# Optimization experiments

Hardware: AMD Instinct MI355X
Metric: run time of the kernel (lower is better)

## Reference

```python
import jax, jax.numpy as jnp
import numpy as np

B, S, D, H = 8, 384, 768, 12
MAX_POS = 512
P = 2 * MAX_POS - 1  # 1023


def setup_inputs() -> dict:
    key = jax.random.key(0)
    ks = jax.random.split(key, 14)
    w = 0.02
    return {
        "x": jax.random.normal(ks[0], (B, S, D), jnp.float32),
        "rel_pos_emb": jax.random.normal(ks[1], (P, D), jnp.float32),
        "Wq": jax.random.normal(ks[2], (D, D), jnp.float32) * w,
        "bq": jax.random.normal(ks[3], (D,), jnp.float32) * w,
        "Wk": jax.random.normal(ks[4], (D, D), jnp.float32) * w,
        "bk": jax.random.normal(ks[5], (D,), jnp.float32) * w,
        "Wv": jax.random.normal(ks[6], (D, D), jnp.float32) * w,
        "bv": jax.random.normal(ks[7], (D,), jnp.float32) * w,
        "q_bias": jax.random.normal(ks[8], (D,), jnp.float32) * w,
        "v_bias": jax.random.normal(ks[9], (D,), jnp.float32) * w,
        "Wpk": jax.random.normal(ks[10], (D, D), jnp.float32) * w,
        "Wpq": jax.random.normal(ks[11], (D, D), jnp.float32) * w,
        "Wo": jax.random.normal(ks[12], (D, D), jnp.float32) * w,
        "bo": jax.random.normal(ks[13], (D,), jnp.float32) * w,
    }


def reference(x, rel_pos_emb, Wq, bq, Wk, bk, Wv, bv, q_bias, v_bias, Wpk, Wpq, Wo, bo):
    b, s, d = x.shape
    dh = d // H
    scale = dh ** -0.5
    # relative position index: rel[i, j] = j - i + MAX_POS - 1
    rel = (jnp.arange(s)[None, :] - jnp.arange(s)[:, None]) + MAX_POS - 1
    emb = rel_pos_emb[rel]                      # [S, S, D]
    q = (x @ Wq + bq + q_bias).reshape(b, s, H, dh)
    k = (x @ Wk + bk).reshape(b, s, H, dh)
    v = (x @ Wv + bv + v_bias).reshape(b, s, H, dh)
    Kp = (emb @ Wpk).reshape(s, s, H, dh)       # pos keys   [i, j, h, d]
    Qp = (emb @ Wpq).reshape(s, s, H, dh)       # pos queries[i, j, h, d]
    c2c = jnp.einsum('bihd,bjhd->bhij', q, k)
    c2p = jnp.einsum('bihd,ijhd->bhij', q, Kp)
    p2c = jnp.einsum('ijhd,bjhd->bhij', Qp, k)
    scores = (c2c + c2p + p2c) * scale          # [B, H, S, S]
    w = jax.nn.softmax(scores, axis=-1)
    out = jnp.einsum('bhij,bjhd->bihd', w, v).reshape(b, s, d)
    return out @ Wo + bo
```

## Files before the change

### kernel.cpp

```cpp
#include <hip/hip_runtime.h>
#include <hip/hip_bf16.h>
#include <math.h>

#define BATCH 8
#define SEQ 384
#define DIM 768
#define NH 12
#define DH 64
#define NPOS 767
#define POS_OFF 128
#define NTOK (BATCH * SEQ)
#define QKN 1536
#define QKVN 2304
#define PN 1536

typedef __attribute__((ext_vector_type(8))) short short8;
typedef __attribute__((ext_vector_type(4))) float floatx4;
typedef unsigned int u32;

__device__ __forceinline__ ushort f2bf(float f) {
    __hip_bfloat16 h = __float2bfloat16(f);
    return *reinterpret_cast<ushort*>(&h);
}
__device__ __forceinline__ float bf2f(ushort u) {
    u32 x = ((u32)u) << 16;
    float f; __builtin_memcpy(&f, &x, 4); return f;
}

__device__ __forceinline__ void gld16(const ushort* g, ushort* l) {
    __builtin_amdgcn_global_load_lds(
        (const __attribute__((address_space(1))) u32*)g,
        (__attribute__((address_space(3))) u32*)l, 16, 0, 0);
}

#define MFMA __builtin_amdgcn_mfma_f32_16x16x32_bf16

__global__ __launch_bounds__(256) void prep(
    const float* W0, const float* W1, const float* W2,
    const float* W3, const float* W4, const float* W5,
    const float* x, const float* rpe,
    ushort* __restrict__ wsT, ushort* __restrict__ xb, ushort* __restrict__ rpeb)
{
    const int tid = threadIdx.x;
    if (blockIdx.z < 6) {
        __shared__ float t[64][65];
        const float* srcs[6] = {W0, W1, W2, W3, W4, W5};
        const float* in = srcs[blockIdx.z];
        ushort* out = wsT + (size_t)blockIdx.z * DIM * DIM;
        const int r0 = blockIdx.y * 64, c0 = blockIdx.x * 64;
        for (int p = 0; p < 16; ++p) {
            int e = tid + p * 256, i = e >> 6, j = e & 63;
            t[i][j] = in[(size_t)(r0 + i) * DIM + c0 + j];
        }
        __syncthreads();
        for (int p = 0; p < 16; ++p) {
            int e = tid + p * 256, i = e >> 6, j = e & 63;
            out[(size_t)(c0 + i) * DIM + r0 + j] = f2bf(t[j][i]);
        }
    } else {
        const int n4x = NTOK * DIM / 4;
        const int n4p = NPOS * DIM / 4;
        const int fb = blockIdx.y * 12 + blockIdx.x;
        for (int idx = fb * 256 + tid; idx < n4x + n4p; idx += 144 * 256) {
            const float* src; ushort* dst; int j;
            if (idx < n4x) { src = x; dst = xb; j = idx; }
            else { src = rpe + (size_t)POS_OFF * DIM; dst = rpeb; j = idx - n4x; }
            float4 f = ((const float4*)src)[j];
            ushort o[4] = {f2bf(f.x), f2bf(f.y), f2bf(f.z), f2bf(f.w)};
            *(uint2*)&dst[(size_t)j * 4] = *(uint2*)o;
        }
    }
}

__global__ __launch_bounds__(256) void proj_all(
    const ushort* __restrict__ xb, const ushort* __restrict__ rpeb,
    const ushort* __restrict__ wsT,
    const float* __restrict__ bq, const float* __restrict__ qbias,
    const float* __restrict__ bk, const float* __restrict__ bv,
    const float* __restrict__ vbias,
    ushort* __restrict__ qk, ushort* __restrict__ vT, ushort* __restrict__ posKQ)
{
    __shared__ ushort As[128 * 64];
    __shared__ ushort Bs[128 * 64];
    const int tid = threadIdx.x;
    const int lane = tid & 63, w = tid >> 6;
    const int id = blockIdx.x;
    const bool qkvP = id < 432;
    const ushort* A; const ushort* Bt; int m0, n0, M;
    if (qkvP) {
        m0 = (id % 24) * 128; n0 = (id / 24) * 128;
        A = xb; Bt = wsT; M = NTOK;
    } else {
        int p = id - 432;
        m0 = (p % 6) * 128; n0 = (p / 6) * 128;
        A = rpeb; Bt = wsT + (size_t)3 * DIM * DIM; M = NPOS;
    }
    const int lr = lane >> 3;
    const int lc = (lane & 7) ^ (lr & 7);
    const ushort* ga[4]; const ushort* gb[4];
#pragma unroll
    for (int p = 0; p < 4; ++p) {
        int row = (w * 4 + p) * 8 + lr;
        int arow = m0 + row; if (arow > M - 1) arow = M - 1;
        ga[p] = A + (size_t)arow * DIM + lc * 8;
        gb[p] = Bt + (size_t)(n0 + row) * DIM + lc * 8;
    }
    floatx4 acc[4][4] = {};
    const int qr = (w >> 1) * 64, qc = (w & 1) * 64;
    const int lm = lane & 15, lk = lane >> 4;
    for (int k0 = 0; k0 < DIM; k0 += 64) {
#pragma unroll
        for (int p = 0; p < 4; ++p) {
            gld16(ga[p], As + (w * 4 + p) * 512);
            gld16(gb[p], Bs + (w * 4 + p) * 512);
            ga[p] += 64; gb[p] += 64;
        }
        __syncthreads();
#pragma unroll
        for (int kk = 0; kk < 2; ++kk) {
            int ch = (kk * 4 + lk) ^ (lm & 7);
            short8 af[4], bf[4];
#pragma unroll
            for (int t = 0; t < 4; ++t) {
                af[t] = *(const short8*)&As[(qr + t * 16 + lm) * 64 + ch * 8];
                bf[t] = *(const short8*)&Bs[(qc + t * 16 + lm) * 64 + ch * 8];
            }
#pragma unroll
            for (int i = 0; i < 4; ++i)
#pragma unroll
                for (int j = 0; j < 4; ++j)
                    acc[i][j] = MFMA(af[i], bf[j], acc[i][j], 0, 0, 0);
        }
        __syncthreads();
    }
    if (qkvP) {
#pragma unroll
        for (int i = 0; i < 4; ++i) {
            int mbase = m0 + qr + i * 16 + (lane >> 4) * 4;
            int bb = mbase / SEQ;
            int s0 = mbase - bb * SEQ;
#pragma unroll
            for (int j = 0; j < 4; ++j) {
                int n = n0 + qc + j * 16 + lm;
                float bs;
                if (n < 768) bs = bq[n] + qbias[n];
                else if (n < QKN) bs = bk[n - 768];
                else bs = bv[n - QKN] + vbias[n - QKN];
                if (n < QKN) {
#pragma unroll
                    for (int r = 0; r < 4; ++r)
                        qk[(size_t)(mbase + r) * QKN + n] = f2bf(acc[i][j][r] + bs);
                } else {
                    int c = n - QKN, h = c >> 6, d = c & 63;
                    ushort tmp[4];
#pragma unroll
                    for (int r = 0; r < 4; ++r) tmp[r] = f2bf(acc[i][j][r] + bs);
                    *(uint2*)&vT[(((size_t)bb * NH + h) * DH + d) * SEQ + s0] = *(uint2*)tmp;
                }
            }
        }
    } else {
#pragma unroll
        for (int i = 0; i < 4; ++i) {
            int mbase = m0 + qr + i * 16 + (lane >> 4) * 4;
#pragma unroll
            for (int j = 0; j < 4; ++j) {
                int n = n0 + qc + j * 16 + lm;
#pragma unroll
                for (int r = 0; r < 4; ++r) {
                    int row = mbase + r;
                    if (row < NPOS)
                        posKQ[(size_t)row * PN + n] = f2bf(acc[i][j][r]);
                }
            }
        }
    }
}

__global__ __launch_bounds__(256) void gemm128x128(
    const ushort* __restrict__ A, const ushort* __restrict__ Bt,
    const float* __restrict__ bias, float* __restrict__ outF,
    int M, int N, int K)
{
    __shared__ ushort As[128 * 64];
    __shared__ ushort Bs[128 * 64];
    const int tid = threadIdx.x;
    const int lane = tid & 63, w = tid >> 6;
    const int n0 = blockIdx.x * 128, m0 = blockIdx.y * 128;
    const int lr = lane >> 3;
    const int lc = (lane & 7) ^ (lr & 7);
    const ushort* ga[4]; const ushort* gb[4];
#pragma unroll
    for (int p = 0; p < 4; ++p) {
        int row = (w * 4 + p) * 8 + lr;
        int arow = m0 + row; if (arow > M - 1) arow = M - 1;
        ga[p] = A + (size_t)arow * K + lc * 8;
        gb[p] = Bt + (size_t)(n0 + row) * K + lc * 8;
    }
    floatx4 acc[4][4] = {};
    const int qr = (w >> 1) * 64, qc = (w & 1) * 64;
    const int lm = lane & 15, lk = lane >> 4;
    for (int k0 = 0; k0 < K; k0 += 64) {
#pragma unroll
        for (int p = 0; p < 4; ++p) {
            gld16(ga[p], As + (w * 4 + p) * 512);
            gld16(gb[p], Bs + (w * 4 + p) * 512);
            ga[p] += 64; gb[p] += 64;
        }
        __syncthreads();
#pragma unroll
        for (int kk = 0; kk < 2; ++kk) {
            int ch = (kk * 4 + lk) ^ (lm & 7);
            short8 af[4], bf[4];
#pragma unroll
            for (int t = 0; t < 4; ++t) {
                af[t] = *(const short8*)&As[(qr + t * 16 + lm) * 64 + ch * 8];
                bf[t] = *(const short8*)&Bs[(qc + t * 16 + lm) * 64 + ch * 8];
            }
#pragma unroll
            for (int i = 0; i < 4; ++i)
#pragma unroll
                for (int j = 0; j < 4; ++j)
                    acc[i][j] = MFMA(af[i], bf[j], acc[i][j], 0, 0, 0);
        }
        __syncthreads();
    }
#pragma unroll
    for (int i = 0; i < 4; ++i) {
        int mbase = m0 + qr + i * 16 + (lane >> 4) * 4;
#pragma unroll
        for (int j = 0; j < 4; ++j) {
            int n = n0 + qc + j * 16 + lm;
            float bs = bias[n];
#pragma unroll
            for (int r = 0; r < 4; ++r) {
                int row = mbase + r;
                if (row < M) outF[(size_t)row * N + n] = acc[i][j][r] + bs;
            }
        }
    }
}

__global__ __launch_bounds__(512, 2) void attn_fused19(
    const ushort* __restrict__ qk, const ushort* __restrict__ vT,
    const ushort* __restrict__ posKQ, ushort* __restrict__ aob)
{
    __shared__ ushort kt[64 * 64];
    __shared__ ushort kps[128 * 64];
    __shared__ ushort cc[64 * 72];
    __shared__ ushort dqs[64 * 72];
    __shared__ ushort dks[64 * 72];

    const int tid = threadIdx.x;
    const int lane = tid & 63, w = tid >> 6;
    const int i0 = blockIdx.x * 64;
    const int h = blockIdx.y, b = blockIdx.z;
    const int lm = lane & 15, lq = lane >> 4;
    const int lr = lane >> 3, l8 = lane & 7;
    const int lc = l8 ^ (lr & 7);

    short8 qf[2];
    {
        const ushort* qr = qk + (size_t)(b * SEQ + i0 + (w >> 1) * 16 + lm) * QKN + h * DH;
        qf[0] = *(const short8*)(qr + lq * 8);
        qf[1] = *(const short8*)(qr + 32 + lq * 8);
    }
    const ushort* kb = qk + 768 + h * DH;
    floatx4 occ[2] = {};
    float rs = 0.f;

    const int t0i = 320 - i0;
    const int tcb = (w & 1) * 4;
    const int tr = w >> 1;

    {
        gld16(kb + (size_t)(b * SEQ + 8 * w + lr) * QKN + lc * 8, kt + w * 512);
        gld16(posKQ + (size_t)(t0i + 16 * w + lr) * PN + h * DH + lc * 8, kps + w * 1024);
        gld16(posKQ + (size_t)(t0i + 16 * w + 8 + lr) * PN + h * DH + lc * 8, kps + w * 1024 + 512);
    }

    for (int jt = 0; jt < 6; ++jt) {
        const int j0 = jt * 64;
        __syncthreads();

        short8 qpf[2];
        {
            const ushort* qpb = posKQ + (size_t)(t0i + j0 + w * 16 + lm) * PN
                                + 768 + h * DH + lq * 8;
            qpf[0] = *(const short8*)(qpb);
            qpf[1] = *(const short8*)(qpb + 32);
        }

        {
            int tjb = (w & 1) * 2;
            floatx4 a0 = {}, a1 = {};
#pragma unroll
            for (int kk = 0; kk < 2; ++kk) {
                int ch = (kk * 4 + lq) ^ (lm & 7);
                short8 b0 = *(const short8*)&kt[(tjb * 16 + lm) * 64 + ch * 8];
                short8 b1 = *(const short8*)&kt[((tjb + 1) * 16 + lm) * 64 + ch * 8];
                a0 = MFMA(qf[kk], b0, a0, 0, 0, 0);
                a1 = MFMA(qf[kk], b1, a1, 0, 0, 0);
            }
#pragma unroll
            for (int r = 0; r < 4; ++r) {
                cc[(tr * 16 + lq * 4 + r) * 72 + tjb * 16 + lm] = f2bf(a0[r]);
                cc[(tr * 16 + lq * 4 + r) * 72 + (tjb + 1) * 16 + lm] = f2bf(a1[r]);
            }
        }
        {
            floatx4 d[4] = {};
#pragma unroll
            for (int kk = 0; kk < 2; ++kk) {
                int ch = (kk * 4 + lq) ^ (lm & 7);
#pragma unroll
                for (int s = 0; s < 4; ++s) {
                    short8 bf = *(const short8*)&kps[((tcb + s) * 16 + lm) * 64 + ch * 8];
                    d[s] = MFMA(qf[kk], bf, d[s], 0, 0, 0);
                }
            }
#pragma unroll
            for (int s = 0; s < 4; ++s) {
                int t = (tcb + s) * 16 + lm;
#pragma unroll
                for (int r = 0; r < 4; ++r) {
                    int i = tr * 16 + lq * 4 + r;
                    int j = t + i - 63;
                    if ((unsigned)j < 64u) dqs[i * 72 + j] = f2bf(d[s][r]);
                }
            }
        }
        {
            floatx4 e[4] = {};
#pragma unroll
            for (int kk = 0; kk < 2; ++kk) {
                int ch = (kk * 4 + lq) ^ (lm & 7);
#pragma unroll
                for (int s = 0; s < 4; ++s) {
                    short8 bf = *(const short8*)&kt[(s * 16 + lm) * 64 + ch * 8];
                    e[s] = MFMA(qpf[kk], bf, e[s], 0, 0, 0);
                }
            }
#pragma unroll
            for (int s = 0; s < 4; ++s) {
                int j = s * 16 + lm;
#pragma unroll
                for (int r = 0; r < 4; ++r) {
                    int t = w * 16 + lq * 4 + r;
                    int i = j - t + 63;
                    if ((unsigned)i < 64u) dks[i * 72 + j] = f2bf(e[s][r]);
                }
            }
        }
        __syncthreads();

        if (jt < 5) {
            int t0n = t0i + j0 + 64;
            gld16(kb + (size_t)(b * SEQ + j0 + 64 + 8 * w + lr) * QKN + lc * 8, kt + w * 512);
            gld16(posKQ + (size_t)(t0n + 16 * w + lr) * PN + h * DH + lc * 8, kps + w * 1024);
            gld16(posKQ + (size_t)(t0n + 16 * w + 8 + lr) * PN + h * DH + lc * 8, kps + w * 1024 + 512);
        }

        {
            const int off = (tr * 16 + lm) * 72 + lq * 8;
            short8 af0, af1;
            float psum = 0.f;
            {
                uint4 c4 = *(const uint4*)&cc[off];
                uint4 q4 = *(const uint4*)&dqs[off];
                uint4 k4 = *(const uint4*)&dks[off];
                const ushort* cu = (const ushort*)&c4;
                const ushort* qu = (const ushort*)&q4;
                const ushort* ku = (const ushort*)&k4;
                ushort pv[8];
#pragma unroll
                for (int c = 0; c < 8; ++c) {
                    float pe = __expf((bf2f(cu[c]) + bf2f(qu[c]) + bf2f(ku[c])) * 0.125f);
                    psum += pe;
                    pv[c] = f2bf(pe);
                }
                af0 = *(const short8*)pv;
            }
            {
                uint4 c4 = *(const uint4*)&cc[off + 32];
                uint4 q4 = *(const uint4*)&dqs[off + 32];
                uint4 k4 = *(const uint4*)&dks[off + 32];
                const ushort* cu = (const ushort*)&c4;
                const ushort* qu = (const ushort*)&q4;
                const ushort* ku = (const ushort*)&k4;
                ushort pv[8];
#pragma unroll
                for (int c = 0; c < 8; ++c) {
                    float pe = __expf((bf2f(cu[c]) + bf2f(qu[c]) + bf2f(ku[c])) * 0.125f);
                    psum += pe;
                    pv[c] = f2bf(pe);
                }
                af1 = *(const short8*)pv;
            }
            psum += __shfl_xor(psum, 16);
            psum += __shfl_xor(psum, 32);
            rs += psum;

            int dtb = (w & 1) * 2;
#pragma unroll
            for (int t2 = 0; t2 < 2; ++t2) {
                int dt = dtb + t2;
                const ushort* vr = vT + ((size_t)(b * NH + h) * DH + dt * 16 + lm) * SEQ + j0;
                short8 vf0 = *(const short8*)(vr + lq * 8);
                short8 vf1 = *(const short8*)(vr + 32 + lq * 8);
                occ[t2] = MFMA(af0, vf0, occ[t2], 0, 0, 0);
                occ[t2] = MFMA(af1, vf1, occ[t2], 0, 0, 0);
            }
        }
    }

    {
        int dtb = (w & 1) * 2;
#pragma unroll
        for (int t2 = 0; t2 < 2; ++t2) {
#pragma unroll
            for (int r = 0; r < 4; ++r) {
                int row = tr * 16 + lq * 4 + r;
                float rsv = __shfl(rs, lq * 4 + r);
                float ov = occ[t2][r] / rsv;
                aob[(size_t)(b * SEQ + i0 + row) * DIM + h * DH + (dtb + t2) * 16 + lm] = f2bf(ov);
            }
        }
    }
}

extern "C" void kernel_launch(void* const* d_in, const int* in_sizes, int n_in,
                              void* d_out, int out_size, void* d_ws, size_t ws_size,
                              hipStream_t stream) {
    const float* x   = (const float*)d_in[0];
    const float* rpe = (const float*)d_in[1];
    const float* Wq  = (const float*)d_in[2];
    const float* bq  = (const float*)d_in[3];
    const float* Wk  = (const float*)d_in[4];
    const float* bk  = (const float*)d_in[5];
    const float* Wv  = (const float*)d_in[6];
    const float* bv  = (const float*)d_in[7];
    const float* qbias = (const float*)d_in[8];
    const float* vbias = (const float*)d_in[9];
    const float* Wpk = (const float*)d_in[10];
    const float* Wpq = (const float*)d_in[11];
    const float* Wo  = (const float*)d_in[12];
    const float* bo  = (const float*)d_in[13];
    float* out = (float*)d_out;

    char* ws = (char*)d_ws;
    ushort* xb    = (ushort*)ws; ws += (size_t)NTOK * DIM * 2;
    ushort* qkbuf = (ushort*)ws; ws += (size_t)NTOK * QKN * 2;
    ushort* vT    = (ushort*)ws; ws += (size_t)NTOK * DIM * 2;
    ushort* aob   = (ushort*)ws; ws += (size_t)NTOK * DIM * 2;
    ushort* rpeb  = (ushort*)ws; ws += (size_t)NPOS * DIM * 2;
    ushort* posKQ = (ushort*)ws; ws += (size_t)NPOS * PN * 2;
    ushort* wsT   = (ushort*)ws; ws += (size_t)6 * DIM * DIM * 2;

    prep<<<dim3(12, 12, 7), dim3(256), 0, stream>>>(
        Wq, Wk, Wv, Wpk, Wpq, Wo, x, rpe, wsT, xb, rpeb);
    proj_all<<<dim3(504), dim3(256), 0, stream>>>(
        xb, rpeb, wsT, bq, qbias, bk, bv, vbias, qkbuf, vT, posKQ);
    attn_fused19<<<dim3(SEQ / 64, NH, BATCH), dim3(512), 0, stream>>>(qkbuf, vT, posKQ, aob);
    gemm128x128<<<dim3(DIM / 128, NTOK / 128), dim3(256), 0, stream>>>(
        aob, wsT + (size_t)5 * DIM * DIM, bo, out, NTOK, DIM, DIM);
}
```

Baseline: 186.4 us.

## Split attention key range across two blocks and combine partials in separate kernel

The attention kernel now processes half of the key sequence per block, doubling the grid, and writes unnormalized fp32 partial outputs and row sums to workspace. A new combine kernel adds the two partials, normalizes by the summed row sums and writes bf16 output for the final projection. This aims to improve CU occupancy and wave balance, at the cost of extra global memory traffic for fp32 partials and an additional kernel launch.

Result: slower. 197.5 us (+6.0%).

```diff
diff --git a/kernel.cpp b/kernel.cpp
--- a/kernel.cpp
+++ b/kernel.cpp
@@ -241,9 +241,10 @@
     }
 }
 
-__global__ __launch_bounds__(512, 2) void attn_fused19(
+__global__ __launch_bounds__(512, 2) void attn_part(
     const ushort* __restrict__ qk, const ushort* __restrict__ vT,
-    const ushort* __restrict__ posKQ, ushort* __restrict__ aob)
+    const ushort* __restrict__ posKQ,
+    float* __restrict__ pO, float* __restrict__ pR)
 {
     __shared__ ushort kt[64 * 64];
     __shared__ ushort kps[128 * 64];
@@ -253,7 +254,8 @@
 
     const int tid = threadIdx.x;
     const int lane = tid & 63, w = tid >> 6;
-    const int i0 = blockIdx.x * 64;
+    const int i0 = (blockIdx.x >> 1) * 64;
+    const int jg = blockIdx.x & 1;
     const int h = blockIdx.y, b = blockIdx.z;
     const int lm = lane & 15, lq = lane >> 4;
     const int lr = lane >> 3, l8 = lane & 7;
@@ -272,15 +274,16 @@
     const int t0i = 320 - i0;
     const int tcb = (w & 1) * 4;
     const int tr = w >> 1;
+    const int jbase = jg * 192;
 
     {
-        gld16(kb + (size_t)(b * SEQ + 8 * w + lr) * QKN + lc * 8, kt + w * 512);
-        gld16(posKQ + (size_t)(t0i + 16 * w + lr) * PN + h * DH + lc * 8, kps + w * 1024);
-        gld16(posKQ + (size_t)(t0i + 16 * w + 8 + lr) * PN + h * DH + lc * 8, kps + w * 1024 + 512);
-    }
-
-    for (int jt = 0; jt < 6; ++jt) {
-        const int j0 = jt * 64;
+        gld16(kb + (size_t)(b * SEQ + jbase + 8 * w + lr) * QKN + lc * 8, kt + w * 512);
+        gld16(posKQ + (size_t)(t0i + jbase + 16 * w + lr) * PN + h * DH + lc * 8, kps + w * 1024);
+        gld16(posKQ + (size_t)(t0i + jbase + 16 * w + 8 + lr) * PN + h * DH + lc * 8, kps + w * 1024 + 512);
+    }
+
+    for (int jt = 0; jt < 3; ++jt) {
+        const int j0 = jbase + jt * 64;
         __syncthreads();
 
         short8 qpf[2];
@@ -354,7 +357,7 @@
         }
         __syncthreads();
 
-        if (jt < 5) {
+        if (jt < 2) {
             int t0n = t0i + j0 + 64;
             gld16(kb + (size_t)(b * SEQ + j0 + 64 + 8 * w + lr) * QKN + lc * 8, kt + w * 512);
             gld16(posKQ + (size_t)(t0n + 16 * w + lr) * PN + h * DH + lc * 8, kps + w * 1024);
@@ -421,12 +424,31 @@
 #pragma unroll
             for (int r = 0; r < 4; ++r) {
                 int row = tr * 16 + lq * 4 + r;
-                float rsv = __shfl(rs, lq * 4 + r);
-                float ov = occ[t2][r] / rsv;
-                aob[(size_t)(b * SEQ + i0 + row) * DIM + h * DH + (dtb + t2) * 16 + lm] = f2bf(ov);
-            }
-        }
-    }
+                pO[((size_t)jg * NTOK + b * SEQ + i0 + row) * DIM + h * DH + (dtb + t2) * 16 + lm]
+                    = occ[t2][r];
+            }
+        }
+        if ((w & 1) == 0 && lq == 0)
+            pR[((size_t)jg * NTOK + b * SEQ + i0 + tr * 16 + lm) * NH + h] = rs;
+    }
+}
+
+__global__ __launch_bounds__(256) void combine(
+    const float* __restrict__ pO, const float* __restrict__ pR,
+    ushort* __restrict__ aob)
+{
+    const int n4 = NTOK * DIM / 4;
+    int idx = blockIdx.x * 256 + threadIdx.x;
+    int e0 = idx * 4;
+    int row = e0 / DIM;
+    int h = (e0 - row * DIM) >> 6;
+    float4 a = ((const float4*)pO)[idx];
+    float4 c = ((const float4*)pO)[idx + n4];
+    float r = pR[row * NH + h] + pR[(NTOK + row) * NH + h];
+    float inv = 1.0f / r;
+    ushort o[4] = { f2bf((a.x + c.x) * inv), f2bf((a.y + c.y) * inv),
+                    f2bf((a.z + c.z) * inv), f2bf((a.w + c.w) * inv) };
+    ((uint2*)aob)[idx] = *(uint2*)o;
 }
 
 extern "C" void kernel_launch(void* const* d_in, const int* in_sizes, int n_in,
@@ -456,12 +478,16 @@
     ushort* rpeb  = (ushort*)ws; ws += (size_t)NPOS * DIM * 2;
     ushort* posKQ = (ushort*)ws; ws += (size_t)NPOS * PN * 2;
     ushort* wsT   = (ushort*)ws; ws += (size_t)6 * DIM * DIM * 2;
+    float*  pO    = (float*)ws;  ws += (size_t)2 * NTOK * DIM * 4;
+    float*  pR    = (float*)ws;  ws += (size_t)2 * NTOK * NH * 4;
 
     prep<<<dim3(12, 12, 7), dim3(256), 0, stream>>>(
         Wq, Wk, Wv, Wpk, Wpq, Wo, x, rpe, wsT, xb, rpeb);
     proj_all<<<dim3(504), dim3(256), 0, stream>>>(
         xb, rpeb, wsT, bq, qbias, bk, bv, vbias, qkbuf, vT, posKQ);
-    attn_fused19<<<dim3(SEQ / 64, NH, BATCH), dim3(512), 0, stream>>>(qkbuf, vT, posKQ, aob);
+    attn_part<<<dim3(12, NH, BATCH), dim3(512), 0, stream>>>(
+        qkbuf, vT, posKQ, pO, pR);
+    combine<<<dim3(NTOK * DIM / 4 / 256), dim3(256), 0, stream>>>(pO, pR, aob);
     gemm128x128<<<dim3(DIM / 128, NTOK / 128), dim3(256), 0, stream>>>(
         aob, wsT + (size_t)5 * DIM * DIM, bo, out, NTOK, DIM, DIM);
 }
```
